# Performance work log

Measured on AMD Instinct MI355X. Metric: run time of the kernel, lower is better.

The kernel has to match this reference:

```python
import jax, jax.numpy as jnp
import numpy as np

T = 256          # total_sequence_length
COND = 192       # condition_size
H = 256          # latent_size
B = 4096         # batch
MEAN = 0.0
STD = 1.0


def setup_inputs() -> dict:
    key = jax.random.key(0)
    ks = jax.random.split(key, 8)
    s = 1.0 / np.sqrt(H)  # PyTorch RNN init scale
    return {
        "cd": jax.random.normal(ks[0], (B, COND), dtype=jnp.float32),
        "prediction": jax.random.normal(ks[1], (B, T - COND), dtype=jnp.float32),
        "w_ih": jax.random.uniform(ks[2], (4 * H, 1), jnp.float32, -s, s),
        "w_hh": jax.random.uniform(ks[3], (4 * H, H), jnp.float32, -s, s),
        "b_ih": jax.random.uniform(ks[4], (4 * H,), jnp.float32, -s, s),
        "b_hh": jax.random.uniform(ks[5], (4 * H,), jnp.float32, -s, s),
        "w_out": jax.random.uniform(ks[6], (1, H), jnp.float32, -s, s),
        "b_out": jax.random.uniform(ks[7], (1,), jnp.float32, -s, s),
    }


def reference(cd, prediction, w_ih, w_hh, b_ih, b_hh, w_out, b_out):
    # concat condition + prediction -> [B, T], normalize
    d_input = jnp.concatenate([cd, prediction.reshape(-1, T - COND)], axis=1)
    d_input = (d_input - MEAN) / STD
    # time-major [T, B]; input_size=1 so x-projection is an outer product
    x = d_input.T  # [T, B]
    # precompute input gates for all timesteps: [T, B, 4H]
    x_gates = x[:, :, None] * w_ih[:, 0][None, None, :] + b_ih

    def step(carry, xg):
        h, c = carry
        gates = xg + h @ w_hh.T + b_hh  # [B, 4H]
        i, f, g, o = jnp.split(gates, 4, axis=1)
        i = jax.nn.sigmoid(i)
        f = jax.nn.sigmoid(f)
        g = jnp.tanh(g)
        o = jax.nn.sigmoid(o)
        c = f * c + i * g
        h = o * jnp.tanh(c)
        return (h, c), None

    h0 = jnp.zeros((B, H), dtype=cd.dtype)
    c0 = jnp.zeros((B, H), dtype=cd.dtype)
    (h_last, _), _ = jax.lax.scan(step, (h0, c0), x_gates)
    # trailing linear + sigmoid on last hidden state -> [B, 1]
    return jax.nn.sigmoid(h_last @ w_out.T + b_out)
```

## Files before the change

### kernel.cpp

```cpp
#include <hip/hip_runtime.h>

#define TT 256
#define CONDL 192
#define PREDL 64
#define HH 256
#define BB 4096
#define BT 16
#define NTHR 512

#define WSC 2032.0f
#define HSC 127.0f
#define SINV (1.0f / (127.0f * 2032.0f))

typedef int i32x4 __attribute__((ext_vector_type(4)));
typedef signed char i8x16 __attribute__((ext_vector_type(16)));
typedef unsigned short u16x4 __attribute__((ext_vector_type(4)));

__device__ __forceinline__ short f2bf(float f) {
  unsigned u = __builtin_bit_cast(unsigned, f);
  unsigned r = (u + 0x7fffu + ((u >> 16) & 1u)) >> 16;
  return (short)r;
}
__device__ __forceinline__ float bf2f(short s) {
  unsigned u = ((unsigned)(unsigned short)s) << 16;
  return __builtin_bit_cast(float, u);
}
__device__ __forceinline__ float bflo(unsigned p) {
  return __builtin_bit_cast(float, p << 16);
}
__device__ __forceinline__ float bfhi(unsigned p) {
  return __builtin_bit_cast(float, p & 0xffff0000u);
}
__device__ __forceinline__ float sig_(float x) {
  return __builtin_amdgcn_rcpf(1.0f + __builtin_amdgcn_exp2f(-1.44269504f * x));
}
__device__ __forceinline__ float tanh_(float x) {
  float e = __builtin_amdgcn_exp2f(2.88539008f * x);
  return 1.0f - 2.0f * __builtin_amdgcn_rcpf(e + 1.0f);
}

__global__ void pack_w(const float* __restrict__ w_hh, signed char* __restrict__ wq) {
  int idx = blockIdx.x * 256 + threadIdx.x;
  int lane = idx & 63;
  int kb = (idx >> 6) & 3;
  int jt = idx >> 8;
  int n = jt * 16 + (lane & 15);
  int k0 = kb * 64 + (lane >> 4) * 16;
  i8x16 v;
#pragma unroll
  for (int j = 0; j < 16; ++j)
    v[j] = (signed char)__float2int_rn(w_hh[n * 256 + k0 + j] * WSC);
  *(i8x16*)(wq + (long)idx * 16) = v;
}

__global__ __launch_bounds__(NTHR, 2)
void lstm_main(const float* __restrict__ cd, const float* __restrict__ pred,
               const float* __restrict__ w_ih, const float* __restrict__ b_ih,
               const float* __restrict__ b_hh, const float* __restrict__ w_out,
               const float* __restrict__ b_out, const signed char* __restrict__ wq,
               float* __restrict__ out) {
  __shared__ __align__(16) signed char h_s[2 * 4096];
  __shared__ __align__(16) short x_s[TT * BT];

  const int tid = threadIdx.x;
  const int lane = tid & 63;
  const int wv = tid >> 6;
  const int r0 = blockIdx.x * BT;
  const int lm = lane & 15;
  const int lq = lane >> 4;
  const int m0 = lq * 4;

  for (int i = tid; i < BT * CONDL; i += NTHR) {
    int r = i / CONDL, t = i % CONDL;
    x_s[t * BT + r] = f2bf(cd[(r0 + r) * CONDL + t]);
  }
  for (int i = tid; i < BT * PREDL; i += NTHR) {
    int r = i / PREDL, t = i % PREDL;
    x_s[(CONDL + t) * BT + r] = f2bf(pred[(r0 + r) * PREDL + t]);
  }
  for (int i = tid; i < 1024; i += NTHR) ((int*)h_s)[i] = 0;

  const i32x4* wq4 = (const i32x4*)wq;
  i32x4 wrq[32];
#pragma unroll
  for (int a = 0; a < 8; ++a) {
    int jt = (a >> 1) * 16 + wv * 2 + (a & 1);
#pragma unroll
    for (int kb = 0; kb < 4; ++kb)
      wrq[a * 4 + kb] = wq4[(jt * 4 + kb) * 64 + lane];
  }
#pragma unroll
  for (int i = 0; i < 32; ++i) asm volatile("" : "+v"(wrq[i]));

  unsigned wbs[8];
#pragma unroll
  for (int a = 0; a < 8; ++a) {
    int j = (a >> 1) * 256 + (wv * 2 + (a & 1)) * 16 + lm;
    unsigned lo = (unsigned short)f2bf(w_ih[j]);
    unsigned hi = (unsigned short)f2bf(b_ih[j] + b_hh[j]);
    wbs[a] = lo | (hi << 16);
  }

  int wbb[2];
#pragma unroll
  for (int i = 0; i < 2; ++i)
    wbb[i] = (wv >> 1) * 1024 + ((wv * 2 + i) & 3) * 256 + lq * 64 + lm;

  float cst[8];
#pragma unroll
  for (int i = 0; i < 8; ++i) cst[i] = 0.f;

  i32x4 zeroi;
  zeroi[0] = 0; zeroi[1] = 0; zeroi[2] = 0; zeroi[3] = 0;

  __syncthreads();

  for (int t = 0; t < TT; ++t) {
    const signed char* hr = h_s + (t & 1) * 4096;
    signed char* hw = h_s + ((t + 1) & 1) * 4096;

    i32x4 acc[8];

    i32x4 af_c = *(const i32x4*)(hr + lane * 16);
#pragma unroll
    for (int kb = 0; kb < 4; ++kb) {
      i32x4 af = af_c;
      if (kb < 3) af_c = *(const i32x4*)(hr + (kb + 1) * 1024 + lane * 16);
      acc[0] = __builtin_amdgcn_mfma_i32_16x16x64_i8(
          af, wrq[0 * 4 + kb], kb ? acc[0] : zeroi, 0, 0, 0);
      acc[1] = __builtin_amdgcn_mfma_i32_16x16x64_i8(
          af, wrq[1 * 4 + kb], kb ? acc[1] : zeroi, 0, 0, 0);
      acc[2] = __builtin_amdgcn_mfma_i32_16x16x64_i8(
          af, wrq[2 * 4 + kb], kb ? acc[2] : zeroi, 0, 0, 0);
      acc[3] = __builtin_amdgcn_mfma_i32_16x16x64_i8(
          af, wrq[3 * 4 + kb], kb ? acc[3] : zeroi, 0, 0, 0);
      acc[4] = __builtin_amdgcn_mfma_i32_16x16x64_i8(
          af, wrq[4 * 4 + kb], kb ? acc[4] : zeroi, 0, 0, 0);
      acc[5] = __builtin_amdgcn_mfma_i32_16x16x64_i8(
          af, wrq[5 * 4 + kb], kb ? acc[5] : zeroi, 0, 0, 0);
      acc[6] = __builtin_amdgcn_mfma_i32_16x16x64_i8(
          af, wrq[6 * 4 + kb], kb ? acc[6] : zeroi, 0, 0, 0);
      acc[7] = __builtin_amdgcn_mfma_i32_16x16x64_i8(
          af, wrq[7 * 4 + kb], kb ? acc[7] : zeroi, 0, 0, 0);
    }

    u16x4 xq = *(const u16x4*)(x_s + t * BT + m0);
    float xr[4];
#pragma unroll
    for (int v = 0; v < 4; ++v) xr[v] = bf2f((short)xq[v]);

#pragma unroll
    for (int i = 0; i < 2; ++i) {
      float wI = bflo(wbs[i]),     bI = bfhi(wbs[i]);
      float wF = bflo(wbs[2 + i]), bF = bfhi(wbs[2 + i]);
      float wG = bflo(wbs[4 + i]), bG = bfhi(wbs[4 + i]);
      float wO = bflo(wbs[6 + i]), bO = bfhi(wbs[6 + i]);
#pragma unroll
      for (int v = 0; v < 4; ++v) {
        float ig = sig_(fmaf((float)acc[i][v],     SINV, fmaf(xr[v], wI, bI)));
        float fg = sig_(fmaf((float)acc[2 + i][v], SINV, fmaf(xr[v], wF, bF)));
        float gg = tanh_(fmaf((float)acc[4 + i][v], SINV, fmaf(xr[v], wG, bG)));
        float og = sig_(fmaf((float)acc[6 + i][v], SINV, fmaf(xr[v], wO, bO)));
        float cn = fg * cst[i * 4 + v] + ig * gg;
        cst[i * 4 + v] = cn;
        float hv = og * tanh_(cn);
        hw[wbb[i] + v * 16] = (signed char)__float2int_rn(hv * HSC);
      }
    }
    __syncthreads();
  }

  const signed char* hf = h_s;
  float bo = b_out[0];
#pragma unroll
  for (int rr = 0; rr < 2; ++rr) {
    int row = wv * 2 + rr;
    float p = 0.f;
#pragma unroll
    for (int c = 0; c < 4; ++c) {
      int k = lane + c * 64;
      int idx = c * 1024 + ((lane >> 4) & 3) * 256 + row * 16 + (lane & 15);
      p += (float)hf[idx] * w_out[k];
    }
#pragma unroll
    for (int off = 32; off > 0; off >>= 1) p += __shfl_down(p, off);
    if (lane == 0) out[r0 + row] = sig_(p * (1.0f / HSC) + bo);
  }
}

extern "C" void kernel_launch(void* const* d_in, const int* in_sizes, int n_in,
                              void* d_out, int out_size, void* d_ws, size_t ws_size,
                              hipStream_t stream) {
  const float* cd    = (const float*)d_in[0];
  const float* pr    = (const float*)d_in[1];
  const float* w_ih  = (const float*)d_in[2];
  const float* w_hh  = (const float*)d_in[3];
  const float* b_ih  = (const float*)d_in[4];
  const float* b_hh  = (const float*)d_in[5];
  const float* w_out = (const float*)d_in[6];
  const float* b_out = (const float*)d_in[7];
  float* out = (float*)d_out;
  signed char* wp = (signed char*)d_ws;

  pack_w<<<64, 256, 0, stream>>>(w_hh, wp);
  lstm_main<<<256, NTHR, 0, stream>>>(cd, pr, w_ih, b_ih, b_hh, w_out, b_out, wp, out);
}
```

Measured before the change: 500.0 us.

## Interleave odd-column MFMAs with even-column gate math and prefold activation constants

The per-step schedule now issues the even-column MFMA chain first, then interleaves the odd-column MFMAs with the elementwise gate computation for the even column, so matrix-core latency overlaps with transcendental work. All four h fragments and the x value are loaded up front. The log2(e) and dequantization scales are folded into fp32 input weights, biases and MFMA scale constants, which removes per-element multiplies and bf16 unpacking. This keeps more fp32 weight and bias values in registers, adding register pressure under the two-blocks-per-CU launch bound.

```diff
diff --git a/kernel.cpp b/kernel.cpp
--- a/kernel.cpp
+++ b/kernel.cpp
@@ -11,6 +11,9 @@
 #define WSC 2032.0f
 #define HSC 127.0f
 #define SINV (1.0f / (127.0f * 2032.0f))
+#define L2E 1.44269504f
+#define CSX (-L2E * SINV)
+#define CGX (2.0f * L2E * SINV)
 
 typedef int i32x4 __attribute__((ext_vector_type(4)));
 typedef signed char i8x16 __attribute__((ext_vector_type(16)));
@@ -24,19 +27,6 @@
 __device__ __forceinline__ float bf2f(short s) {
   unsigned u = ((unsigned)(unsigned short)s) << 16;
   return __builtin_bit_cast(float, u);
-}
-__device__ __forceinline__ float bflo(unsigned p) {
-  return __builtin_bit_cast(float, p << 16);
-}
-__device__ __forceinline__ float bfhi(unsigned p) {
-  return __builtin_bit_cast(float, p & 0xffff0000u);
-}
-__device__ __forceinline__ float sig_(float x) {
-  return __builtin_amdgcn_rcpf(1.0f + __builtin_amdgcn_exp2f(-1.44269504f * x));
-}
-__device__ __forceinline__ float tanh_(float x) {
-  float e = __builtin_amdgcn_exp2f(2.88539008f * x);
-  return 1.0f - 2.0f * __builtin_amdgcn_rcpf(e + 1.0f);
 }
 
 __global__ void pack_w(const float* __restrict__ w_hh, signed char* __restrict__ wq) {
@@ -92,13 +82,14 @@
 #pragma unroll
   for (int i = 0; i < 32; ++i) asm volatile("" : "+v"(wrq[i]));
 
-  unsigned wbs[8];
+  float wf_[8], bf_[8];
 #pragma unroll
   for (int a = 0; a < 8; ++a) {
-    int j = (a >> 1) * 256 + (wv * 2 + (a & 1)) * 16 + lm;
-    unsigned lo = (unsigned short)f2bf(w_ih[j]);
-    unsigned hi = (unsigned short)f2bf(b_ih[j] + b_hh[j]);
-    wbs[a] = lo | (hi << 16);
+    int g = a >> 1;
+    int j = g * 256 + (wv * 2 + (a & 1)) * 16 + lm;
+    float fac = (g == 2) ? (2.0f * L2E) : -L2E;
+    wf_[a] = w_ih[j] * fac;
+    bf_[a] = (b_ih[j] + b_hh[j]) * fac;
   }
 
   int wbb[2];
@@ -119,54 +110,60 @@
     const signed char* hr = h_s + (t & 1) * 4096;
     signed char* hw = h_s + ((t + 1) & 1) * 4096;
 
+    i32x4 af0 = *(const i32x4*)(hr + 0 * 1024 + lane * 16);
+    i32x4 af1 = *(const i32x4*)(hr + 1 * 1024 + lane * 16);
+    i32x4 af2 = *(const i32x4*)(hr + 2 * 1024 + lane * 16);
+    i32x4 af3 = *(const i32x4*)(hr + 3 * 1024 + lane * 16);
+    u16x4 xq = *(const u16x4*)(x_s + t * BT + m0);
+
+    float xr[4];
+#pragma unroll
+    for (int v = 0; v < 4; ++v) xr[v] = bf2f((short)xq[v]);
+
     i32x4 acc[8];
 
-    i32x4 af_c = *(const i32x4*)(hr + lane * 16);
-#pragma unroll
-    for (int kb = 0; kb < 4; ++kb) {
-      i32x4 af = af_c;
-      if (kb < 3) af_c = *(const i32x4*)(hr + (kb + 1) * 1024 + lane * 16);
-      acc[0] = __builtin_amdgcn_mfma_i32_16x16x64_i8(
-          af, wrq[0 * 4 + kb], kb ? acc[0] : zeroi, 0, 0, 0);
-      acc[1] = __builtin_amdgcn_mfma_i32_16x16x64_i8(
-          af, wrq[1 * 4 + kb], kb ? acc[1] : zeroi, 0, 0, 0);
-      acc[2] = __builtin_amdgcn_mfma_i32_16x16x64_i8(
-          af, wrq[2 * 4 + kb], kb ? acc[2] : zeroi, 0, 0, 0);
-      acc[3] = __builtin_amdgcn_mfma_i32_16x16x64_i8(
-          af, wrq[3 * 4 + kb], kb ? acc[3] : zeroi, 0, 0, 0);
-      acc[4] = __builtin_amdgcn_mfma_i32_16x16x64_i8(
-          af, wrq[4 * 4 + kb], kb ? acc[4] : zeroi, 0, 0, 0);
-      acc[5] = __builtin_amdgcn_mfma_i32_16x16x64_i8(
-          af, wrq[5 * 4 + kb], kb ? acc[5] : zeroi, 0, 0, 0);
-      acc[6] = __builtin_amdgcn_mfma_i32_16x16x64_i8(
-          af, wrq[6 * 4 + kb], kb ? acc[6] : zeroi, 0, 0, 0);
-      acc[7] = __builtin_amdgcn_mfma_i32_16x16x64_i8(
-          af, wrq[7 * 4 + kb], kb ? acc[7] : zeroi, 0, 0, 0);
+#define MQ(AF, KB, ODD)                                                        \
+    acc[0 + ODD] = __builtin_amdgcn_mfma_i32_16x16x64_i8(                      \
+        AF, wrq[(0 + ODD) * 4 + KB], KB ? acc[0 + ODD] : zeroi, 0, 0, 0);      \
+    acc[2 + ODD] = __builtin_amdgcn_mfma_i32_16x16x64_i8(                      \
+        AF, wrq[(2 + ODD) * 4 + KB], KB ? acc[2 + ODD] : zeroi, 0, 0, 0);      \
+    acc[4 + ODD] = __builtin_amdgcn_mfma_i32_16x16x64_i8(                      \
+        AF, wrq[(4 + ODD) * 4 + KB], KB ? acc[4 + ODD] : zeroi, 0, 0, 0);      \
+    acc[6 + ODD] = __builtin_amdgcn_mfma_i32_16x16x64_i8(                      \
+        AF, wrq[(6 + ODD) * 4 + KB], KB ? acc[6 + ODD] : zeroi, 0, 0, 0);
+
+    MQ(af0, 0, 0) MQ(af1, 1, 0) MQ(af2, 2, 0) MQ(af3, 3, 0)
+
+#define ELEMC(I, V)                                                            \
+    {                                                                          \
+      float aI = (float)acc[0 + I][V];                                         \
+      float aF = (float)acc[2 + I][V];                                         \
+      float aG = (float)acc[4 + I][V];                                         \
+      float aO = (float)acc[6 + I][V];                                         \
+      float ig = __builtin_amdgcn_rcpf(                                        \
+          1.0f + __builtin_amdgcn_exp2f(fmaf(aI, CSX, fmaf(xr[V], wf_[0 + I], bf_[0 + I])))); \
+      float fg = __builtin_amdgcn_rcpf(                                        \
+          1.0f + __builtin_amdgcn_exp2f(fmaf(aF, CSX, fmaf(xr[V], wf_[2 + I], bf_[2 + I])))); \
+      float gg = fmaf(-2.0f, __builtin_amdgcn_rcpf(                            \
+          1.0f + __builtin_amdgcn_exp2f(fmaf(aG, CGX, fmaf(xr[V], wf_[4 + I], bf_[4 + I])))), 1.0f); \
+      float og = __builtin_amdgcn_rcpf(                                        \
+          1.0f + __builtin_amdgcn_exp2f(fmaf(aO, CSX, fmaf(xr[V], wf_[6 + I], bf_[6 + I])))); \
+      float cn = fmaf(fg, cst[I * 4 + V], ig * gg);                            \
+      cst[I * 4 + V] = cn;                                                     \
+      float tc = fmaf(-2.0f, __builtin_amdgcn_rcpf(                            \
+          1.0f + __builtin_amdgcn_exp2f(2.0f * L2E * cn)), 1.0f);              \
+      hw[wbb[I] + V * 16] = (signed char)__float2int_rn(og * tc * HSC);        \
     }
 
-    u16x4 xq = *(const u16x4*)(x_s + t * BT + m0);
-    float xr[4];
-#pragma unroll
-    for (int v = 0; v < 4; ++v) xr[v] = bf2f((short)xq[v]);
-
-#pragma unroll
-    for (int i = 0; i < 2; ++i) {
-      float wI = bflo(wbs[i]),     bI = bfhi(wbs[i]);
-      float wF = bflo(wbs[2 + i]), bF = bfhi(wbs[2 + i]);
-      float wG = bflo(wbs[4 + i]), bG = bfhi(wbs[4 + i]);
-      float wO = bflo(wbs[6 + i]), bO = bfhi(wbs[6 + i]);
-#pragma unroll
-      for (int v = 0; v < 4; ++v) {
-        float ig = sig_(fmaf((float)acc[i][v],     SINV, fmaf(xr[v], wI, bI)));
-        float fg = sig_(fmaf((float)acc[2 + i][v], SINV, fmaf(xr[v], wF, bF)));
-        float gg = tanh_(fmaf((float)acc[4 + i][v], SINV, fmaf(xr[v], wG, bG)));
-        float og = sig_(fmaf((float)acc[6 + i][v], SINV, fmaf(xr[v], wO, bO)));
-        float cn = fg * cst[i * 4 + v] + ig * gg;
-        cst[i * 4 + v] = cn;
-        float hv = og * tanh_(cn);
-        hw[wbb[i] + v * 16] = (signed char)__float2int_rn(hv * HSC);
-      }
-    }
+    MQ(af0, 0, 1) ELEMC(0, 0)
+    MQ(af1, 1, 1) ELEMC(0, 1)
+    MQ(af2, 2, 1) ELEMC(0, 2)
+    MQ(af3, 3, 1) ELEMC(0, 3)
+
+    ELEMC(1, 0) ELEMC(1, 1) ELEMC(1, 2) ELEMC(1, 3)
+
+#undef MQ
+#undef ELEMC
     __syncthreads();
   }
 
@@ -184,7 +181,10 @@
     }
 #pragma unroll
     for (int off = 32; off > 0; off >>= 1) p += __shfl_down(p, off);
-    if (lane == 0) out[r0 + row] = sig_(p * (1.0f / HSC) + bo);
+    if (lane == 0) {
+      float z = p * (1.0f / HSC) + bo;
+      out[r0 + row] = __builtin_amdgcn_rcpf(1.0f + __builtin_amdgcn_exp2f(-L2E * z));
+    }
   }
 }
 
```

Measured after the change: 485.9 us. -2.8%, faster.

## Split gate work across 16 waves and fuse LSTM activations with shared reciprocals

Applied to the files above, without the earlier changes.

Doubles the block to 1024 threads so each wave owns one hidden column tile (4 MFMA accumulators instead of 8), which halves per-thread register weight storage and per-step serial work. The gate nonlinearities are rewritten algebraically: the log2(e) scale is folded into the input weights, biases and accumulator scale, and the sigmoid/tanh combinations for c and h are merged so each element needs two reciprocals instead of five. The exp argument for the cell tanh is clamped to avoid overflow. More waves per block means the per-step barrier synchronises twice as many waves, and the fused formulas may lose a little precision.

```diff
diff --git a/kernel.cpp b/kernel.cpp
--- a/kernel.cpp
+++ b/kernel.cpp
@@ -6,11 +6,14 @@
 #define HH 256
 #define BB 4096
 #define BT 16
-#define NTHR 512
+#define NTHR 1024
 
 #define WSC 2032.0f
 #define HSC 127.0f
 #define SINV (1.0f / (127.0f * 2032.0f))
+#define L2E 1.44269504f
+#define CSX (-L2E * SINV)
+#define CGX (2.0f * L2E * SINV)
 
 typedef int i32x4 __attribute__((ext_vector_type(4)));
 typedef signed char i8x16 __attribute__((ext_vector_type(16)));
@@ -25,18 +28,8 @@
   unsigned u = ((unsigned)(unsigned short)s) << 16;
   return __builtin_bit_cast(float, u);
 }
-__device__ __forceinline__ float bflo(unsigned p) {
-  return __builtin_bit_cast(float, p << 16);
-}
-__device__ __forceinline__ float bfhi(unsigned p) {
-  return __builtin_bit_cast(float, p & 0xffff0000u);
-}
 __device__ __forceinline__ float sig_(float x) {
-  return __builtin_amdgcn_rcpf(1.0f + __builtin_amdgcn_exp2f(-1.44269504f * x));
-}
-__device__ __forceinline__ float tanh_(float x) {
-  float e = __builtin_amdgcn_exp2f(2.88539008f * x);
-  return 1.0f - 2.0f * __builtin_amdgcn_rcpf(e + 1.0f);
+  return __builtin_amdgcn_rcpf(1.0f + __builtin_amdgcn_exp2f(-L2E * x));
 }
 
 __global__ void pack_w(const float* __restrict__ w_hh, signed char* __restrict__ wq) {
@@ -53,7 +46,7 @@
   *(i8x16*)(wq + (long)idx * 16) = v;
 }
 
-__global__ __launch_bounds__(NTHR, 2)
+__global__ __launch_bounds__(NTHR, 4)
 void lstm_main(const float* __restrict__ cd, const float* __restrict__ pred,
                const float* __restrict__ w_ih, const float* __restrict__ b_ih,
                const float* __restrict__ b_hh, const float* __restrict__ w_out,
@@ -81,34 +74,31 @@
   for (int i = tid; i < 1024; i += NTHR) ((int*)h_s)[i] = 0;
 
   const i32x4* wq4 = (const i32x4*)wq;
-  i32x4 wrq[32];
+  i32x4 wrq[16];
 #pragma unroll
-  for (int a = 0; a < 8; ++a) {
-    int jt = (a >> 1) * 16 + wv * 2 + (a & 1);
+  for (int g = 0; g < 4; ++g) {
+    int jt = g * 16 + wv;
 #pragma unroll
     for (int kb = 0; kb < 4; ++kb)
-      wrq[a * 4 + kb] = wq4[(jt * 4 + kb) * 64 + lane];
+      wrq[g * 4 + kb] = wq4[(jt * 4 + kb) * 64 + lane];
   }
 #pragma unroll
-  for (int i = 0; i < 32; ++i) asm volatile("" : "+v"(wrq[i]));
+  for (int i = 0; i < 16; ++i) asm volatile("" : "+v"(wrq[i]));
 
-  unsigned wbs[8];
+  float wf_[4], bf_[4];
 #pragma unroll
-  for (int a = 0; a < 8; ++a) {
-    int j = (a >> 1) * 256 + (wv * 2 + (a & 1)) * 16 + lm;
-    unsigned lo = (unsigned short)f2bf(w_ih[j]);
-    unsigned hi = (unsigned short)f2bf(b_ih[j] + b_hh[j]);
-    wbs[a] = lo | (hi << 16);
+  for (int g = 0; g < 4; ++g) {
+    int j = g * 256 + wv * 16 + lm;
+    float fac = (g == 2) ? (2.0f * L2E) : -L2E;
+    wf_[g] = w_ih[j] * fac;
+    bf_[g] = (b_ih[j] + b_hh[j]) * fac;
   }
 
-  int wbb[2];
+  const int wbb = (wv >> 2) * 1024 + (wv & 3) * 256 + lq * 64 + lm;
+
+  float cst[4];
 #pragma unroll
-  for (int i = 0; i < 2; ++i)
-    wbb[i] = (wv >> 1) * 1024 + ((wv * 2 + i) & 3) * 256 + lq * 64 + lm;
-
-  float cst[8];
-#pragma unroll
-  for (int i = 0; i < 8; ++i) cst[i] = 0.f;
+  for (int i = 0; i < 4; ++i) cst[i] = 0.f;
 
   i32x4 zeroi;
   zeroi[0] = 0; zeroi[1] = 0; zeroi[2] = 0; zeroi[3] = 0;
@@ -119,7 +109,7 @@
     const signed char* hr = h_s + (t & 1) * 4096;
     signed char* hw = h_s + ((t + 1) & 1) * 4096;
 
-    i32x4 acc[8];
+    i32x4 acc[4];
 
     i32x4 af_c = *(const i32x4*)(hr + lane * 16);
 #pragma unroll
@@ -134,14 +124,6 @@
           af, wrq[2 * 4 + kb], kb ? acc[2] : zeroi, 0, 0, 0);
       acc[3] = __builtin_amdgcn_mfma_i32_16x16x64_i8(
           af, wrq[3 * 4 + kb], kb ? acc[3] : zeroi, 0, 0, 0);
-      acc[4] = __builtin_amdgcn_mfma_i32_16x16x64_i8(
-          af, wrq[4 * 4 + kb], kb ? acc[4] : zeroi, 0, 0, 0);
-      acc[5] = __builtin_amdgcn_mfma_i32_16x16x64_i8(
-          af, wrq[5 * 4 + kb], kb ? acc[5] : zeroi, 0, 0, 0);
-      acc[6] = __builtin_amdgcn_mfma_i32_16x16x64_i8(
-          af, wrq[6 * 4 + kb], kb ? acc[6] : zeroi, 0, 0, 0);
-      acc[7] = __builtin_amdgcn_mfma_i32_16x16x64_i8(
-          af, wrq[7 * 4 + kb], kb ? acc[7] : zeroi, 0, 0, 0);
     }
 
     u16x4 xq = *(const u16x4*)(x_s + t * BT + m0);
@@ -150,31 +132,35 @@
     for (int v = 0; v < 4; ++v) xr[v] = bf2f((short)xq[v]);
 
 #pragma unroll
-    for (int i = 0; i < 2; ++i) {
-      float wI = bflo(wbs[i]),     bI = bfhi(wbs[i]);
-      float wF = bflo(wbs[2 + i]), bF = bfhi(wbs[2 + i]);
-      float wG = bflo(wbs[4 + i]), bG = bfhi(wbs[4 + i]);
-      float wO = bflo(wbs[6 + i]), bO = bfhi(wbs[6 + i]);
-#pragma unroll
-      for (int v = 0; v < 4; ++v) {
-        float ig = sig_(fmaf((float)acc[i][v],     SINV, fmaf(xr[v], wI, bI)));
-        float fg = sig_(fmaf((float)acc[2 + i][v], SINV, fmaf(xr[v], wF, bF)));
-        float gg = tanh_(fmaf((float)acc[4 + i][v], SINV, fmaf(xr[v], wG, bG)));
-        float og = sig_(fmaf((float)acc[6 + i][v], SINV, fmaf(xr[v], wO, bO)));
-        float cn = fg * cst[i * 4 + v] + ig * gg;
-        cst[i * 4 + v] = cn;
-        float hv = og * tanh_(cn);
-        hw[wbb[i] + v * 16] = (signed char)__float2int_rn(hv * HSC);
-      }
+    for (int v = 0; v < 4; ++v) {
+      float aI = (float)acc[0][v];
+      float aF = (float)acc[1][v];
+      float aG = (float)acc[2][v];
+      float aO = (float)acc[3][v];
+      float xi = xr[v];
+      float eI = __builtin_amdgcn_exp2f(fmaf(aI, CSX, fmaf(xi, wf_[0], bf_[0])));
+      float eF = __builtin_amdgcn_exp2f(fmaf(aF, CSX, fmaf(xi, wf_[1], bf_[1])));
+      float eG = __builtin_amdgcn_exp2f(fmaf(aG, CGX, fmaf(xi, wf_[2], bf_[2])));
+      float eO = __builtin_amdgcn_exp2f(fmaf(aO, CSX, fmaf(xi, wf_[3], bf_[3])));
+      float A_ = 1.0f + eI, F_ = 1.0f + eF, G_ = 1.0f + eG, O_ = 1.0f + eO;
+      float AG = A_ * G_;
+      float num = fmaf(G_ - 2.0f, F_, cst[v] * AG);
+      float r1 = __builtin_amdgcn_rcpf(F_ * AG);
+      float cn = num * r1;
+      cst[v] = cn;
+      float eC = __builtin_amdgcn_exp2f(fminf(cn * (2.0f * L2E), 126.0f));
+      float C2 = 1.0f + eC;
+      float r2 = __builtin_amdgcn_rcpf(O_ * C2);
+      float h127 = fmaf(HSC, C2, -2.0f * HSC) * r2;
+      hw[wbb + v * 16] = (signed char)__float2int_rn(h127);
     }
     __syncthreads();
   }
 
   const signed char* hf = h_s;
   float bo = b_out[0];
-#pragma unroll
-  for (int rr = 0; rr < 2; ++rr) {
-    int row = wv * 2 + rr;
+  {
+    int row = wv;
     float p = 0.f;
 #pragma unroll
     for (int c = 0; c < 4; ++c) {
```

After: 418.8 us (median of 2 runs). 16.2% less time.
